# Optimization experiments

Measured on AMD Instinct MI355X. Metric: run time of the kernel, lower is better.

Reference implementation:

```python
import jax, jax.numpy as jnp
import numpy as np

HIDDEN = 512
OUT = 16
T = 90  # forecast_length


def setup_inputs() -> dict:
    key = jax.random.key(0)
    ks = jax.random.split(key, 8)
    B, S, H, O = 64, 256, HIDDEN, OUT
    lim1 = 1.0 / np.sqrt(H)
    return {
        "latent": jax.random.normal(ks[0], (B, S, H), dtype=jnp.float32),
        "W1": jax.random.uniform(ks[1], (H, H), jnp.float32, -lim1, lim1),
        "b1": jax.random.uniform(ks[2], (H,), jnp.float32, -lim1, lim1),
        "W2": jax.random.uniform(ks[3], (H, H), jnp.float32, -lim1, lim1),
        "b2": jax.random.uniform(ks[4], (H,), jnp.float32, -lim1, lim1),
        "Wout": jax.random.uniform(ks[5], (O, H), jnp.float32, -lim1, lim1),
        "bout": jax.random.uniform(ks[6], (O,), jnp.float32, -lim1, lim1),
        "pos_enc": jax.random.normal(ks[7], (1, T, H), dtype=jnp.float32) * 0.02,
    }


def reference(latent, W1, b1, W2, b2, Wout, bout, pos_enc):
    # state: (B, S, H); pos_enc[0]: (T, H) scanned per step.
    def step(state, pe_t):
        x = state + pe_t  # broadcast (H,) over (B, S, H)
        h = jax.nn.gelu(jnp.einsum('bsh,kh->bsk', x, W1) + b1, approximate=False)
        h = jnp.einsum('bsh,kh->bsk', h, W2) + b2
        state = state + h  # residual
        out = jnp.einsum('bsh,oh->bso', state, Wout) + bout
        return state, out

    _, outs = jax.lax.scan(step, latent, pos_enc[0])  # outs: (T, B, S, O)
    Tn, B, S, O = outs.shape
    # torch.cat(outputs, dim=-2): concatenate step outputs along the -2 axis (t-major)
    return jnp.transpose(outs, (1, 0, 2, 3)).reshape(B, Tn * S, O)
```

## Files before the change

### kernel.cpp

```cpp
#include <hip/hip_runtime.h>
#include <hip/hip_bf16.h>

typedef __attribute__((ext_vector_type(8))) short short8;
typedef __attribute__((ext_vector_type(4))) float f32x4;

#define HID 512
#define T_STEPS 90
#define RBLK 64
#define NBLK 256

__device__ __forceinline__ unsigned short f2bf(float x) {
  unsigned int u = __float_as_uint(x);
  u = u + 0x7FFFu + ((u >> 16) & 1u);
  return (unsigned short)(u >> 16);
}
__device__ __forceinline__ float bf2f(unsigned short s) {
  return __uint_as_float(((unsigned int)s) << 16);
}

__device__ __forceinline__ float gelu_f(float x) {
  float u = fabsf(x) * 0.70710678118654752f;
  float d = fmaf(0.3275911f, u, 1.0f);
  float t; asm("v_rcp_f32 %0, %1" : "=v"(t) : "v"(d));
  float poly = t * (0.254829592f + t * (-0.284496736f + t * (1.421413741f +
               t * (-1.453152027f + t * 1.061405429f))));
  float m = -u * u * 1.44269504088896f;
  float ex; asm("v_exp_f32 %0, %1" : "=v"(ex) : "v"(m));
  float e = 1.0f - poly * ex;
  e = copysignf(e, x);
  return 0.5f * x * (1.0f + e);
}

__global__ void prep_convert(const float* __restrict__ W1, const float* __restrict__ W2,
                             const float* __restrict__ Wout, unsigned short* __restrict__ wbf) {
  int i = blockIdx.x * blockDim.x + threadIdx.x;
  if (i >= 532480) return;
  float v;
  if (i < 262144) v = W1[i];
  else if (i < 524288) v = W2[i - 262144];
  else v = Wout[i - 524288];
  wbf[i] = f2bf(v);
}

__global__ void prep_corr(const float* __restrict__ pos, const float* __restrict__ bout,
                          const unsigned short* __restrict__ Woutbf, float* __restrict__ corr) {
  int i = blockIdx.x * blockDim.x + threadIdx.x;
  if (i >= T_STEPS * 16) return;
  int t = i >> 4, o = i & 15;
  float s = 0.f;
  if (t < T_STEPS - 1) {
    const float* pe = pos + (t + 1) * HID;
    for (int h = 0; h < HID; ++h) s += pe[h] * bf2f(Woutbf[o * HID + h]);
  }
  corr[i] = bout[o] - s;
}

__device__ __forceinline__ void gemm_tile(const unsigned short* Alds,
                                          const unsigned short* __restrict__ Wbf,
                                          f32x4 (&acc)[4][4],
                                          int cb, int lh, int lq,
                                          const int abase, const int axor) {
  const unsigned short* wp0 = Wbf + (cb + 0 * 16 + lh) * HID + lq * 8;
  const unsigned short* wp1 = Wbf + (cb + 1 * 16 + lh) * HID + lq * 8;
  const unsigned short* wp2 = Wbf + (cb + 2 * 16 + lh) * HID + lq * 8;
  const unsigned short* wp3 = Wbf + (cb + 3 * 16 + lh) * HID + lq * 8;
  short8 buf[4][4];
#pragma unroll
  for (int d = 0; d < 3; ++d) {
    buf[d][0] = *(const short8*)(wp0 + d * 32);
    buf[d][1] = *(const short8*)(wp1 + d * 32);
    buf[d][2] = *(const short8*)(wp2 + d * 32);
    buf[d][3] = *(const short8*)(wp3 + d * 32);
  }
#pragma unroll
  for (int kk = 0; kk < 16; ++kk) {
    if (kk + 3 < 16) {
      const int s = (kk + 3) & 3;
      buf[s][0] = *(const short8*)(wp0 + (kk + 3) * 32);
      buf[s][1] = *(const short8*)(wp1 + (kk + 3) * 32);
      buf[s][2] = *(const short8*)(wp2 + (kk + 3) * 32);
      buf[s][3] = *(const short8*)(wp3 + (kk + 3) * 32);
    }
    const int c = kk & 3;
    short8 af[4];
#pragma unroll
    for (int mt = 0; mt < 4; ++mt)
      af[mt] = *(const short8*)(Alds + (((mt * 8192) + abase + kk * 32) ^ axor));
#pragma unroll
    for (int mt = 0; mt < 4; ++mt)
#pragma unroll
      for (int nt = 0; nt < 4; ++nt)
        acc[mt][nt] = __builtin_amdgcn_mfma_f32_16x16x32_bf16(af[mt], buf[c][nt], acc[mt][nt], 0, 0, 0);
  }
}

__global__ __launch_bounds__(512, 2) void fd_main(
    const float* __restrict__ latent, const float* __restrict__ b1,
    const float* __restrict__ b2, const float* __restrict__ pos,
    const unsigned short* __restrict__ W1bf, const unsigned short* __restrict__ W2bf,
    const unsigned short* __restrict__ Woutbf, const float* __restrict__ corr,
    unsigned int* __restrict__ gbar, float* __restrict__ out) {
  __shared__ __align__(16) unsigned short Xs[RBLK * HID];
  __shared__ __align__(16) unsigned short Hs[RBLK * HID];
  const int tid = threadIdx.x;
  const int w = tid >> 6;
  const int l = tid & 63;
  const int lh = l & 15, lq = l >> 4;
  const int cb = w << 6;
  const int cbl = cb + lh;
  const int rowBase = blockIdx.x * RBLK;
  const int abase = lh * HID + lq * 8;
  const int axor = (lh & 7) << 3;

  float b1v[4], b2v[4];
#pragma unroll
  for (int nt = 0; nt < 4; ++nt) { b1v[nt] = b1[cbl + nt * 16]; b2v[nt] = b2[cbl + nt * 16]; }

  f32x4 st[4][4];
#pragma unroll
  for (int mt = 0; mt < 4; ++mt)
#pragma unroll
    for (int nt = 0; nt < 4; ++nt) {
#pragma unroll
      for (int r = 0; r < 4; ++r)
        st[mt][nt][r] = latent[(size_t)(rowBase + mt * 16 + lq * 4 + r) * HID + cbl + nt * 16];
    }

  {
    float pev[4];
#pragma unroll
    for (int nt = 0; nt < 4; ++nt) pev[nt] = pos[cbl + nt * 16];
#pragma unroll
    for (int mt = 0; mt < 4; ++mt)
#pragma unroll
      for (int nt = 0; nt < 4; ++nt)
#pragma unroll
        for (int r = 0; r < 4; ++r) {
          int row = mt * 16 + lq * 4 + r;
          int idx = ((row << 9) + cbl + nt * 16) ^ ((row & 7) << 3);
          Xs[idx] = f2bf(st[mt][nt][r] + pev[nt]);
        }
  }
  __syncthreads();

  const unsigned short* woutp = Woutbf + lh * HID + lq * 8;

  for (int t = 0; t < T_STEPS; ++t) {
    f32x4 a1[4][4];
#pragma unroll
    for (int mt = 0; mt < 4; ++mt)
#pragma unroll
      for (int nt = 0; nt < 4; ++nt)
        a1[mt][nt] = (f32x4){b1v[nt], b1v[nt], b1v[nt], b1v[nt]};
    gemm_tile(Xs, W1bf, a1, cb, lh, lq, abase, axor);

#pragma unroll
    for (int mt = 0; mt < 4; ++mt)
#pragma unroll
      for (int nt = 0; nt < 4; ++nt)
#pragma unroll
        for (int r = 0; r < 4; ++r) {
          float g = gelu_f(a1[mt][nt][r]);
          int row = mt * 16 + lq * 4 + r;
          int idx = ((row << 9) + cbl + nt * 16) ^ ((row & 7) << 3);
          Hs[idx] = f2bf(g);
        }
    __syncthreads();

#pragma unroll
    for (int mt = 0; mt < 4; ++mt)
#pragma unroll
      for (int nt = 0; nt < 4; ++nt)
        st[mt][nt] += b2v[nt];
    gemm_tile(Hs, W2bf, st, cb, lh, lq, abase, axor);

    {
      float pev[4] = {0.f, 0.f, 0.f, 0.f};
      if (t < T_STEPS - 1) {
#pragma unroll
        for (int nt = 0; nt < 4; ++nt) pev[nt] = pos[(t + 1) * HID + cbl + nt * 16];
      }
#pragma unroll
      for (int mt = 0; mt < 4; ++mt)
#pragma unroll
        for (int nt = 0; nt < 4; ++nt)
#pragma unroll
          for (int r = 0; r < 4; ++r) {
            int row = mt * 16 + lq * 4 + r;
            int idx = ((row << 9) + cbl + nt * 16) ^ ((row & 7) << 3);
            Xs[idx] = f2bf(st[mt][nt][r] + pev[nt]);
          }
    }
    __syncthreads();

    if (w < 4) {
      const int mt = w;
      float cv = corr[t * 16 + lh];
      f32x4 ao = {cv, cv, cv, cv};
#pragma unroll
      for (int kk = 0; kk < 16; ++kk) {
        short8 af = *(const short8*)(Xs + (((mt * 8192) + abase + kk * 32) ^ axor));
        short8 bfr = *(const short8*)(woutp + kk * 32);
        ao = __builtin_amdgcn_mfma_f32_16x16x32_bf16(af, bfr, ao, 0, 0, 0);
      }
#pragma unroll
      for (int r = 0; r < 4; ++r) {
        int row = rowBase + mt * 16 + lq * 4 + r;
        int bb = row >> 8, ss = row & 255;
        out[(size_t)((bb * T_STEPS + t) * 256 + ss) * 16 + lh] = ao[r];
      }
    } else if (tid == 448) {
      unsigned int target = 256u * (unsigned int)(t + 1);
      __hip_atomic_fetch_add(gbar, 1u, __ATOMIC_RELAXED, __HIP_MEMORY_SCOPE_AGENT);
      for (int p = 0; p < 1000; ++p) {
        unsigned int v = __hip_atomic_fetch_add(gbar, 0u, __ATOMIC_RELAXED, __HIP_MEMORY_SCOPE_AGENT);
        if (v >= target) break;
        __builtin_amdgcn_s_sleep(4);
      }
    }
    __syncthreads();
  }
}

extern "C" void kernel_launch(void* const* d_in, const int* in_sizes, int n_in,
                              void* d_out, int out_size, void* d_ws, size_t ws_size,
                              hipStream_t stream) {
  const float* latent = (const float*)d_in[0];
  const float* W1 = (const float*)d_in[1];
  const float* b1 = (const float*)d_in[2];
  const float* W2 = (const float*)d_in[3];
  const float* b2 = (const float*)d_in[4];
  const float* Wout = (const float*)d_in[5];
  const float* bout = (const float*)d_in[6];
  const float* pos = (const float*)d_in[7];

  unsigned short* wbf = (unsigned short*)d_ws;
  unsigned short* W1bf = wbf;
  unsigned short* W2bf = wbf + 262144;
  unsigned short* Woutbf = wbf + 524288;
  float* corr = (float*)(wbf + 532480);
  unsigned int* gbar = (unsigned int*)((char*)d_ws + 1070720);

  hipMemsetAsync(gbar, 0, 4, stream);
  prep_convert<<<2080, 256, 0, stream>>>(W1, W2, Wout, wbf);
  prep_corr<<<6, 256, 0, stream>>>(pos, bout, Woutbf, corr);
  fd_main<<<NBLK, 512, 0, stream>>>(latent, b1, b2, pos, W1bf, W2bf, Woutbf, corr,
                                    gbar, (float*)d_out);
}
```

Before: 9.817 ms.

## Pre-swizzle bf16 weights into MFMA fragment order for coalesced loads

The prep kernel now writes W1, W2 and Wout in MFMA B-fragment order, so each lane reads one contiguous short8 and a wave reads a fully coalesced 1 KB chunk. Before, each lane gathered 16 bytes from rows strided by 1 KB. The main GEMM prefetches weight fragments two k-steps ahead with a 3-slot ring instead of the earlier 3-deep, 4-slot scheme. The grid barrier spin now uses an atomic load instead of fetch_add(0) and allows 2000 polls before giving up.

```diff
diff --git a/kernel.cpp b/kernel.cpp
--- a/kernel.cpp
+++ b/kernel.cpp
@@ -31,74 +31,75 @@
   return 0.5f * x * (1.0f + e);
 }
 
-__global__ void prep_convert(const float* __restrict__ W1, const float* __restrict__ W2,
-                             const float* __restrict__ Wout, unsigned short* __restrict__ wbf) {
-  int i = blockIdx.x * blockDim.x + threadIdx.x;
-  if (i >= 532480) return;
-  float v;
-  if (i < 262144) v = W1[i];
-  else if (i < 524288) v = W2[i - 262144];
-  else v = Wout[i - 524288];
-  wbf[i] = f2bf(v);
+__global__ void prep_frag(const float* __restrict__ W1, const float* __restrict__ W2,
+                          const float* __restrict__ Wout, unsigned short* __restrict__ dst) {
+  int s = blockIdx.x * blockDim.x + threadIdx.x;
+  if (s >= 66560) return;
+  const float* src; int local; unsigned short* out;
+  if (s < 32768)       { src = W1;   local = s;          out = dst; }
+  else if (s < 65536)  { src = W2;   local = s - 32768;  out = dst + 262144; }
+  else                 { src = Wout; local = s - 65536;  out = dst + 524288; }
+  int c, g, l;
+  if (s < 65536) { c = local >> 11; g = (local >> 6) & 31; l = local & 63; }
+  else           { c = local >> 6;  g = 0;                 l = local & 63; }
+  int col = g * 16 + (l & 15);
+  int h0 = c * 32 + (l >> 4) * 8;
+  const float* p = src + (size_t)col * HID + h0;
+  unsigned short* q = out + (size_t)local * 8;
+#pragma unroll
+  for (int e = 0; e < 8; ++e) q[e] = f2bf(p[e]);
 }
 
 __global__ void prep_corr(const float* __restrict__ pos, const float* __restrict__ bout,
-                          const unsigned short* __restrict__ Woutbf, float* __restrict__ corr) {
+                          const float* __restrict__ Wout, float* __restrict__ corr) {
   int i = blockIdx.x * blockDim.x + threadIdx.x;
   if (i >= T_STEPS * 16) return;
   int t = i >> 4, o = i & 15;
   float s = 0.f;
   if (t < T_STEPS - 1) {
     const float* pe = pos + (t + 1) * HID;
-    for (int h = 0; h < HID; ++h) s += pe[h] * bf2f(Woutbf[o * HID + h]);
+    for (int h = 0; h < HID; ++h) s += pe[h] * bf2f(f2bf(Wout[o * HID + h]));
   }
   corr[i] = bout[o] - s;
 }
 
-__device__ __forceinline__ void gemm_tile(const unsigned short* Alds,
-                                          const unsigned short* __restrict__ Wbf,
-                                          f32x4 (&acc)[4][4],
-                                          int cb, int lh, int lq,
-                                          const int abase, const int axor) {
-  const unsigned short* wp0 = Wbf + (cb + 0 * 16 + lh) * HID + lq * 8;
-  const unsigned short* wp1 = Wbf + (cb + 1 * 16 + lh) * HID + lq * 8;
-  const unsigned short* wp2 = Wbf + (cb + 2 * 16 + lh) * HID + lq * 8;
-  const unsigned short* wp3 = Wbf + (cb + 3 * 16 + lh) * HID + lq * 8;
-  short8 buf[4][4];
-#pragma unroll
-  for (int d = 0; d < 3; ++d) {
-    buf[d][0] = *(const short8*)(wp0 + d * 32);
-    buf[d][1] = *(const short8*)(wp1 + d * 32);
-    buf[d][2] = *(const short8*)(wp2 + d * 32);
-    buf[d][3] = *(const short8*)(wp3 + d * 32);
-  }
-#pragma unroll
-  for (int kk = 0; kk < 16; ++kk) {
-    if (kk + 3 < 16) {
-      const int s = (kk + 3) & 3;
-      buf[s][0] = *(const short8*)(wp0 + (kk + 3) * 32);
-      buf[s][1] = *(const short8*)(wp1 + (kk + 3) * 32);
-      buf[s][2] = *(const short8*)(wp2 + (kk + 3) * 32);
-      buf[s][3] = *(const short8*)(wp3 + (kk + 3) * 32);
-    }
-    const int c = kk & 3;
+__device__ __forceinline__ void gemm_reg(const unsigned short* Alds,
+                                         const short8* __restrict__ Wstg,
+                                         f32x4 (&acc)[4][4],
+                                         const int fo ,
+                                         const int abase, const int axor) {
+  short8 pre[3][4];
+#pragma unroll
+  for (int d = 0; d < 2; ++d)
+#pragma unroll
+    for (int nt = 0; nt < 4; ++nt)
+      pre[d][nt] = Wstg[(size_t)d * 2048 + fo + nt * 64];
+#pragma unroll
+  for (int c = 0; c < 16; ++c) {
+    if (c + 2 < 16) {
+      const int sl = (c + 2) % 3;
+#pragma unroll
+      for (int nt = 0; nt < 4; ++nt)
+        pre[sl][nt] = Wstg[(size_t)(c + 2) * 2048 + fo + nt * 64];
+    }
+    const int cu = c % 3;
     short8 af[4];
 #pragma unroll
     for (int mt = 0; mt < 4; ++mt)
-      af[mt] = *(const short8*)(Alds + (((mt * 8192) + abase + kk * 32) ^ axor));
-#pragma unroll
-    for (int mt = 0; mt < 4; ++mt)
-#pragma unroll
-      for (int nt = 0; nt < 4; ++nt)
-        acc[mt][nt] = __builtin_amdgcn_mfma_f32_16x16x32_bf16(af[mt], buf[c][nt], acc[mt][nt], 0, 0, 0);
+      af[mt] = *(const short8*)(Alds + (((mt * 8192) + abase + c * 32) ^ axor));
+#pragma unroll
+    for (int mt = 0; mt < 4; ++mt)
+#pragma unroll
+      for (int nt = 0; nt < 4; ++nt)
+        acc[mt][nt] = __builtin_amdgcn_mfma_f32_16x16x32_bf16(af[mt], pre[cu][nt], acc[mt][nt], 0, 0, 0);
   }
 }
 
 __global__ __launch_bounds__(512, 2) void fd_main(
     const float* __restrict__ latent, const float* __restrict__ b1,
     const float* __restrict__ b2, const float* __restrict__ pos,
-    const unsigned short* __restrict__ W1bf, const unsigned short* __restrict__ W2bf,
-    const unsigned short* __restrict__ Woutbf, const float* __restrict__ corr,
+    const short8* __restrict__ W1f, const short8* __restrict__ W2f,
+    const short8* __restrict__ Woutf, const float* __restrict__ corr,
     unsigned int* __restrict__ gbar, float* __restrict__ out) {
   __shared__ __align__(16) unsigned short Xs[RBLK * HID];
   __shared__ __align__(16) unsigned short Hs[RBLK * HID];
@@ -108,9 +109,11 @@
   const int lh = l & 15, lq = l >> 4;
   const int cb = w << 6;
   const int cbl = cb + lh;
-  const int rowBase = blockIdx.x * RBLK;
+  const int bid = blockIdx.x;
+  const int rowBase = bid * RBLK;
   const int abase = lh * HID + lq * 8;
   const int axor = (lh & 7) << 3;
+  const int fo = w * 256 + l;
 
   float b1v[4], b2v[4];
 #pragma unroll
@@ -143,8 +146,6 @@
   }
   __syncthreads();
 
-  const unsigned short* woutp = Woutbf + lh * HID + lq * 8;
-
   for (int t = 0; t < T_STEPS; ++t) {
     f32x4 a1[4][4];
 #pragma unroll
@@ -152,7 +153,7 @@
 #pragma unroll
       for (int nt = 0; nt < 4; ++nt)
         a1[mt][nt] = (f32x4){b1v[nt], b1v[nt], b1v[nt], b1v[nt]};
-    gemm_tile(Xs, W1bf, a1, cb, lh, lq, abase, axor);
+    gemm_reg(Xs, W1f, a1, fo, abase, axor);
 
 #pragma unroll
     for (int mt = 0; mt < 4; ++mt)
@@ -172,7 +173,7 @@
 #pragma unroll
       for (int nt = 0; nt < 4; ++nt)
         st[mt][nt] += b2v[nt];
-    gemm_tile(Hs, W2bf, st, cb, lh, lq, abase, axor);
+    gemm_reg(Hs, W2f, st, fo, abase, axor);
 
     {
       float pev[4] = {0.f, 0.f, 0.f, 0.f};
@@ -197,11 +198,14 @@
       const int mt = w;
       float cv = corr[t * 16 + lh];
       f32x4 ao = {cv, cv, cv, cv};
+      short8 po[3];
+#pragma unroll
+      for (int d = 0; d < 2; ++d) po[d] = Woutf[d * 64 + l];
 #pragma unroll
       for (int kk = 0; kk < 16; ++kk) {
+        if (kk + 2 < 16) po[(kk + 2) % 3] = Woutf[(kk + 2) * 64 + l];
         short8 af = *(const short8*)(Xs + (((mt * 8192) + abase + kk * 32) ^ axor));
-        short8 bfr = *(const short8*)(woutp + kk * 32);
-        ao = __builtin_amdgcn_mfma_f32_16x16x32_bf16(af, bfr, ao, 0, 0, 0);
+        ao = __builtin_amdgcn_mfma_f32_16x16x32_bf16(af, po[kk % 3], ao, 0, 0, 0);
       }
 #pragma unroll
       for (int r = 0; r < 4; ++r) {
@@ -212,8 +216,8 @@
     } else if (tid == 448) {
       unsigned int target = 256u * (unsigned int)(t + 1);
       __hip_atomic_fetch_add(gbar, 1u, __ATOMIC_RELAXED, __HIP_MEMORY_SCOPE_AGENT);
-      for (int p = 0; p < 1000; ++p) {
-        unsigned int v = __hip_atomic_fetch_add(gbar, 0u, __ATOMIC_RELAXED, __HIP_MEMORY_SCOPE_AGENT);
+      for (int p = 0; p < 2000; ++p) {
+        unsigned int v = __hip_atomic_load(gbar, __ATOMIC_RELAXED, __HIP_MEMORY_SCOPE_AGENT);
         if (v >= target) break;
         __builtin_amdgcn_s_sleep(4);
       }
@@ -235,15 +239,15 @@
   const float* pos = (const float*)d_in[7];
 
   unsigned short* wbf = (unsigned short*)d_ws;
-  unsigned short* W1bf = wbf;
-  unsigned short* W2bf = wbf + 262144;
-  unsigned short* Woutbf = wbf + 524288;
+  const short8* W1f = (const short8*)wbf;
+  const short8* W2f = (const short8*)(wbf + 262144);
+  const short8* Woutf = (const short8*)(wbf + 524288);
   float* corr = (float*)(wbf + 532480);
   unsigned int* gbar = (unsigned int*)((char*)d_ws + 1070720);
 
   hipMemsetAsync(gbar, 0, 4, stream);
-  prep_convert<<<2080, 256, 0, stream>>>(W1, W2, Wout, wbf);
-  prep_corr<<<6, 256, 0, stream>>>(pos, bout, Woutbf, corr);
-  fd_main<<<NBLK, 512, 0, stream>>>(latent, b1, b2, pos, W1bf, W2bf, Woutbf, corr,
+  prep_frag<<<260, 256, 0, stream>>>(W1, W2, Wout, wbf);
+  prep_corr<<<6, 256, 0, stream>>>(pos, bout, Wout, corr);
+  fd_main<<<NBLK, 512, 0, stream>>>(latent, b1, b2, pos, W1f, W2f, Woutf, corr,
                                     gbar, (float*)d_out);
 }
```

Measured after the change: 11.37 ms. 15.8% more time.
